# Optimization experiments

Hardware: AMD Instinct MI355X
Metric: run time of the kernel (lower is better)

The kernel has to match this reference:

```python
import jax, jax.numpy as jnp
import numpy as np

D_MODEL = 1024
D_STATE = 16
BATCH = 2
SEQ = 2048


def setup_inputs() -> dict:
    key = jax.random.key(0)
    k1, k2, k3, k4, k5 = jax.random.split(key, 5)
    x = jax.random.normal(k1, (BATCH, SEQ, D_MODEL), dtype=jnp.float32)
    log_A_diag = jax.random.normal(k2, (D_MODEL, D_STATE), dtype=jnp.float32)
    B_w = jax.random.normal(k3, (D_STATE, D_MODEL), dtype=jnp.float32) / np.sqrt(D_MODEL)
    C_w = jax.random.normal(k4, (D_MODEL, D_STATE), dtype=jnp.float32) / np.sqrt(D_STATE)
    D_vec = jax.random.normal(k5, (D_MODEL,), dtype=jnp.float32)
    return {"x": x, "log_A_diag": log_A_diag, "B_w": B_w, "C_w": C_w, "D_vec": D_vec}


def reference(x, log_A_diag, B_w, C_w, D_vec):
    # x: (B, L, D)
    B, L, D = x.shape
    pad = 2 * L
    A_bar = jnp.exp(-jnp.exp(log_A_diag))          # (D, S), in (0, 1)
    B_t = jnp.einsum('bld,sd->bls', x, B_w)        # B projection: (B, L, S)
    k_idx = jnp.arange(L, dtype=x.dtype)
    kernel = A_bar[..., None] ** k_idx             # (D, S, L) exponential kernel
    # zero-padded FFT convolution along time axis
    kernel_fft = jnp.fft.rfft(kernel, n=pad, axis=-1)                 # (D, S, L+1)
    B_fft = jnp.fft.rfft(B_t.transpose(0, 2, 1), n=pad, axis=-1)      # (B, S, L+1)
    conv_fft = kernel_fft[None] * B_fft[:, None]                      # (B, D, S, L+1)
    conv = jnp.fft.irfft(conv_fft, n=pad, axis=-1)[..., :L]           # (B, D, S, L)
    # C projection fused over state dim; equivalent to permute->einsum('blds,ds->bld')
    y = jnp.einsum('bdsl,ds->bld', conv, C_w)
    y = y + D_vec[None, None, :] * x               # skip connection
    return y  # dropout is identity in eval mode
```

## Files before the change

### kernel.cpp

```cpp
#include <hip/hip_runtime.h>

#define D_MODEL 1024
#define D_STATE 16
#define BATCH   2
#define SEQ     2048
#define CHUNK   32
#define NCHUNK  (SEQ / CHUNK)
#define NGRP    (SEQ / 4)
#define Q       8
#define SBLEN   (SEQ / Q)
#define SBGRP   (SBLEN / 4)
#define SBCHK   (SBLEN / CHUNK)

__global__ __launch_bounds__(256) void k_bt(const float* __restrict__ x,
                                            const float* __restrict__ Bw,
                                            float* __restrict__ bt,
                                            float* __restrict__ btg) {
    const int t    = threadIdx.x;
    const int wave = t >> 6;
    const int lane = t & 63;

    float4 bw[4][4];
    const float* bwp = Bw + (wave * 4) * D_MODEL + lane * 16;
#pragma unroll
    for (int i = 0; i < 4; ++i)
#pragma unroll
        for (int k = 0; k < 4; ++k)
            bw[i][k] = *(const float4*)(bwp + i * D_MODEL + k * 4);

    const int ROWS = (BATCH * SEQ) / gridDim.x;
    const int row0 = blockIdx.x * ROWS;
    for (int r = 0; r < ROWS; ++r) {
        const int row = row0 + r;
        const float* xr = x + (size_t)row * D_MODEL + lane * 16;
        float4 xv[4];
#pragma unroll
        for (int k = 0; k < 4; ++k) xv[k] = *(const float4*)(xr + k * 4);

        float acc[4] = {0.f, 0.f, 0.f, 0.f};
#pragma unroll
        for (int i = 0; i < 4; ++i) {
#pragma unroll
            for (int k = 0; k < 4; ++k) {
                acc[i] += xv[k].x * bw[i][k].x;
                acc[i] += xv[k].y * bw[i][k].y;
                acc[i] += xv[k].z * bw[i][k].z;
                acc[i] += xv[k].w * bw[i][k].w;
            }
        }
#pragma unroll
        for (int m = 1; m < 64; m <<= 1) {
#pragma unroll
            for (int i = 0; i < 4; ++i) acc[i] += __shfl_xor(acc[i], m, 64);
        }
        if (lane == 0) {
            *(float4*)(bt + (size_t)row * D_STATE + wave * 4) =
                make_float4(acc[0], acc[1], acc[2], acc[3]);
            const int b = row >> 11;
            const int l = row & (SEQ - 1);
            float* p = btg + (((size_t)(b * NGRP + (l >> 2)) * D_STATE + wave * 4) << 2) + (l & 3);
#pragma unroll
            for (int i = 0; i < 4; ++i) p[i * 4] = acc[i];
        }
    }
}

__global__ __launch_bounds__(256) void k_scan(const float* __restrict__ btg,
                                              const float* __restrict__ logA,
                                              float* __restrict__ carry) {
    const int blk = blockIdx.x;
    const int b   = blk >> 9;
    const int dp  = blk & 511;
    const int t   = threadIdx.x;
    const int q   = t >> 5;
    const int ds  = t & 31;
    const int s   = ds & 15;
    const int d   = dp * 2 + (ds >> 4);

    const float A  = expf(-expf(logA[d * D_STATE + s]));
    const float A2 = A * A,    A4 = A2 * A2;
    const float A8 = A4 * A4,  A16 = A8 * A8,  A32 = A16 * A16;
    const float A64 = A32 * A32, A128 = A64 * A64, A256 = A128 * A128;

    const float4* bp = (const float4*)btg + ((size_t)b * NGRP + q * SBGRP) * D_STATE + s;

    float localC[SBCHK];
    float h = 0.f;
#pragma unroll
    for (int k = 0; k < SBCHK; ++k) {
        localC[k] = h;
#pragma unroll
        for (int gg = 0; gg < CHUNK / 4; ++gg) {
            const float4 v = bp[(size_t)(k * (CHUNK / 4) + gg) * D_STATE];
            h = h * A4 + (((v.x * A + v.y) * A + v.z) * A + v.w);
        }
    }

    __shared__ float Fs[32][Q + 1];
    Fs[ds][q] = h;
    __syncthreads();

    float H = 0.f;
    for (int p = 0; p < q; ++p) H = H * A256 + Fs[ds][p];

    float fac = H;
    size_t ci = (((size_t)(b * NCHUNK + q * SBCHK)) * D_MODEL + d) * D_STATE + s;
#pragma unroll
    for (int k = 0; k < SBCHK; ++k) {
        carry[ci] = localC[k] + fac;
        fac *= A32;
        ci += (size_t)D_MODEL * D_STATE;
    }
}

__global__ __launch_bounds__(256) void k_final(const float* __restrict__ x,
                                               const float* __restrict__ logA,
                                               const float* __restrict__ Cw,
                                               const float* __restrict__ Dv,
                                               const float* __restrict__ bt,
                                               const float* __restrict__ carry,
                                               float* __restrict__ y) {
    const int blk = blockIdx.x;
    const int dt  = blk & 3;
    const int c   = (blk >> 2) & (NCHUNK - 1);
    const int b   = blk >> 8;
    const int t   = threadIdx.x;
    const int d   = dt * 256 + t;

    float A[D_STATE], C[D_STATE], h[D_STATE];
    const float* lp = logA + (size_t)d * D_STATE;
    const float* cp = Cw + (size_t)d * D_STATE;
    const float* hp = carry + ((size_t)(b * NCHUNK + c) * D_MODEL + d) * D_STATE;
#pragma unroll
    for (int s = 0; s < D_STATE; ++s) {
        A[s] = expf(-expf(lp[s]));
        C[s] = cp[s];
        h[s] = hp[s];
    }
    const float dv = Dv[d];

    const float* btrow = bt + (size_t)(b * SEQ + c * CHUNK) * D_STATE;
    const size_t rowbase = (size_t)(b * SEQ + c * CHUNK) * D_MODEL + d;
    const float* xp = x + rowbase;
    float*       yp = y + rowbase;

#pragma unroll 4
    for (int j = 0; j < CHUNK; ++j) {
        float acc = dv * xp[(size_t)j * D_MODEL];
#pragma unroll
        for (int s = 0; s < D_STATE; ++s) {
            h[s] = A[s] * h[s] + btrow[j * D_STATE + s];
            acc += C[s] * h[s];
        }
        yp[(size_t)j * D_MODEL] = acc;
    }
}

extern "C" void kernel_launch(void* const* d_in, const int* in_sizes, int n_in,
                              void* d_out, int out_size, void* d_ws, size_t ws_size,
                              hipStream_t stream) {
    const float* x    = (const float*)d_in[0];
    const float* logA = (const float*)d_in[1];
    const float* Bw   = (const float*)d_in[2];
    const float* Cw   = (const float*)d_in[3];
    const float* Dv   = (const float*)d_in[4];
    float* y = (float*)d_out;

    float* bt    = (float*)d_ws;
    float* btg   = bt  + (size_t)BATCH * SEQ * D_STATE;
    float* carry = btg + (size_t)BATCH * SEQ * D_STATE;

    hipLaunchKernelGGL(k_bt,    dim3(512), dim3(256), 0, stream, x, Bw, bt, btg);
    hipLaunchKernelGGL(k_scan,  dim3(BATCH * (D_MODEL / 2)), dim3(256), 0, stream, btg, logA, carry);
    hipLaunchKernelGGL(k_final, dim3(BATCH * NCHUNK * (D_MODEL / 256)), dim3(256), 0, stream, x, logA, Cw, Dv, bt, carry, y);
}
```

Measured before the change: 102.5 us.

## Split chunk scan into local scan with shared-memory staging and carry-fix kernel

The fused scan kernel is split into two kernels. The first stages a sub-block of the grouped B projection into shared memory once per block and shares it across 16 d channels. It writes local chunk carries and per-sub-block final states to global memory. A second kernel combines the prefix of sub-block states and adds the correction into carry in place. This removes repeated global reads of btg across d, at the cost of an extra launch and a read-modify-write pass over most of the carry array.

```diff
diff --git a/kernel.cpp b/kernel.cpp
--- a/kernel.cpp
+++ b/kernel.cpp
@@ -65,49 +65,76 @@
     }
 }
 
-__global__ __launch_bounds__(256) void k_scan(const float* __restrict__ btg,
-                                              const float* __restrict__ logA,
-                                              float* __restrict__ carry) {
+__global__ __launch_bounds__(256) void k_scan_local(const float* __restrict__ btg,
+                                                    const float* __restrict__ logA,
+                                                    float* __restrict__ carry,
+                                                    float* __restrict__ F) {
     const int blk = blockIdx.x;
+    const int dt  = blk & 63;
+    const int q   = (blk >> 6) & 7;
     const int b   = blk >> 9;
-    const int dp  = blk & 511;
     const int t   = threadIdx.x;
-    const int q   = t >> 5;
-    const int ds  = t & 31;
-    const int s   = ds & 15;
-    const int d   = dp * 2 + (ds >> 4);
+    const int s   = t & 15;
+    const int dl  = t >> 4;
+    const int d   = dt * 16 + dl;
+
+    __shared__ float sb[SBLEN * D_STATE];
+    {
+        const float4* src = (const float4*)(btg + (size_t)(b * NGRP + q * SBGRP) * (D_STATE * 4));
+        float4* dst = (float4*)sb;
+#pragma unroll
+        for (int i = 0; i < 4; ++i) dst[t + i * 256] = src[t + i * 256];
+    }
+    __syncthreads();
 
     const float A  = expf(-expf(logA[d * D_STATE + s]));
-    const float A2 = A * A,    A4 = A2 * A2;
-    const float A8 = A4 * A4,  A16 = A8 * A8,  A32 = A16 * A16;
-    const float A64 = A32 * A32, A128 = A64 * A64, A256 = A128 * A128;
-
-    const float4* bp = (const float4*)btg + ((size_t)b * NGRP + q * SBGRP) * D_STATE + s;
-
-    float localC[SBCHK];
+    const float A2 = A * A, A4 = A2 * A2;
+
+    const float4* sb4 = (const float4*)sb;
     float h = 0.f;
+    size_t ci = ((size_t)(b * NCHUNK + q * SBCHK) * D_MODEL + d) * D_STATE + s;
 #pragma unroll
     for (int k = 0; k < SBCHK; ++k) {
-        localC[k] = h;
+        carry[ci] = h;
+        ci += (size_t)D_MODEL * D_STATE;
 #pragma unroll
         for (int gg = 0; gg < CHUNK / 4; ++gg) {
-            const float4 v = bp[(size_t)(k * (CHUNK / 4) + gg) * D_STATE];
+            const float4 v = sb4[(k * (CHUNK / 4) + gg) * D_STATE + s];
             h = h * A4 + (((v.x * A + v.y) * A + v.z) * A + v.w);
         }
     }
-
-    __shared__ float Fs[32][Q + 1];
-    Fs[ds][q] = h;
-    __syncthreads();
+    F[((size_t)(b * Q + q) * D_MODEL + d) * D_STATE + s] = h;
+}
+
+__global__ __launch_bounds__(256) void k_fix(const float* __restrict__ logA,
+                                             const float* __restrict__ F,
+                                             float* __restrict__ carry) {
+    const int blk = blockIdx.x;
+    const int dt  = blk & 63;
+    const int q   = ((blk >> 6) % 7) + 1;
+    const int b   = blk / 448;
+    const int t   = threadIdx.x;
+    const int s   = t & 15;
+    const int dl  = t >> 4;
+    const int d   = dt * 16 + dl;
+
+    const float A = expf(-expf(logA[d * D_STATE + s]));
+    float A32 = A;
+#pragma unroll
+    for (int i = 0; i < 5; ++i) A32 *= A32;
+    float A256 = A32;
+#pragma unroll
+    for (int i = 0; i < 3; ++i) A256 *= A256;
 
     float H = 0.f;
-    for (int p = 0; p < q; ++p) H = H * A256 + Fs[ds][p];
+    for (int p = 0; p < q; ++p)
+        H = H * A256 + F[((size_t)(b * Q + p) * D_MODEL + d) * D_STATE + s];
 
     float fac = H;
-    size_t ci = (((size_t)(b * NCHUNK + q * SBCHK)) * D_MODEL + d) * D_STATE + s;
+    size_t ci = ((size_t)(b * NCHUNK + q * SBCHK) * D_MODEL + d) * D_STATE + s;
 #pragma unroll
     for (int k = 0; k < SBCHK; ++k) {
-        carry[ci] = localC[k] + fac;
+        carry[ci] += fac;
         fac *= A32;
         ci += (size_t)D_MODEL * D_STATE;
     }
@@ -167,10 +194,12 @@
     float* y = (float*)d_out;
 
     float* bt    = (float*)d_ws;
-    float* btg   = bt  + (size_t)BATCH * SEQ * D_STATE;
-    float* carry = btg + (size_t)BATCH * SEQ * D_STATE;
-
-    hipLaunchKernelGGL(k_bt,    dim3(512), dim3(256), 0, stream, x, Bw, bt, btg);
-    hipLaunchKernelGGL(k_scan,  dim3(BATCH * (D_MODEL / 2)), dim3(256), 0, stream, btg, logA, carry);
-    hipLaunchKernelGGL(k_final, dim3(BATCH * NCHUNK * (D_MODEL / 256)), dim3(256), 0, stream, x, logA, Cw, Dv, bt, carry, y);
-}
+    float* btg   = bt    + (size_t)BATCH * SEQ * D_STATE;
+    float* carry = btg   + (size_t)BATCH * SEQ * D_STATE;
+    float* F     = carry + (size_t)BATCH * NCHUNK * D_MODEL * D_STATE;
+
+    hipLaunchKernelGGL(k_bt,         dim3(512), dim3(256), 0, stream, x, Bw, bt, btg);
+    hipLaunchKernelGGL(k_scan_local, dim3(BATCH * Q * 64), dim3(256), 0, stream, btg, logA, carry, F);
+    hipLaunchKernelGGL(k_fix,        dim3(BATCH * 7 * 64), dim3(256), 0, stream, logA, F, carry);
+    hipLaunchKernelGGL(k_final,      dim3(BATCH * NCHUNK * (D_MODEL / 256)), dim3(256), 0, stream, x, logA, Cw, Dv, bt, carry, y);
+}
```

Measured after the change: 103.1 us. Within noise of the previous version (+0.5%).
